# Performance work log

Hardware: AMD Instinct MI355X
Metric: run time of the kernel (lower is better)

The kernel has to match this reference:

```python
import jax, jax.numpy as jnp
import numpy as np

L, U, D_IN, D_OUT, B = 6, 256, 784, 10, 32768  # num_layers, units, input_dim, output_dim, batch


def setup_inputs() -> dict:
    key = jax.random.key(0)
    ks = jax.random.split(key, 7)
    s = jnp.float32(0.05)  # keras 'random_normal' initializer stddev
    return {
        "x": jax.random.normal(ks[0], (B, D_IN), jnp.float32),
        "W_in": jax.random.normal(ks[1], (D_IN, U), jnp.float32) * s,
        "b_in": jax.random.normal(ks[2], (U,), jnp.float32) * s,
        "B0": jax.random.normal(ks[3], (L, U, U), jnp.float32) * s,   # per-layer B0
        "q": jax.random.normal(ks[4], (L, U), jnp.float32) * s,       # per-layer q
        "W_out": jax.random.normal(ks[5], (U, D_OUT), jnp.float32) * s,
        "b_out": jax.random.normal(ks[6], (D_OUT,), jnp.float32) * s,
    }


def reference(x, W_in, b_in, B0, q, W_out, b_out):
    u = W_in.shape[1]
    v0 = (x @ W_in + b_in).T          # (u, B)
    v1 = jnp.tanh(v0)                  # activation of layer 0 applied once before the loop

    def step(carry, params):
        v0, v1 = carry
        B0_l, q_l = params
        z = jnp.zeros((u, u), B0_l.dtype)
        # skew-symmetric block system [[0, B0], [-B0^T, 0]]
        A = jnp.block([[z, B0_l], [-B0_l.T, z]])           # (2u, 2u)
        rhs = jnp.concatenate([v0 + q_l[:, None], v1], 0)   # (2u, B)
        sol = jnp.linalg.solve(A, rhs)
        return (sol[:u], sol[u:]), None

    (v0, v1), _ = jax.lax.scan(step, (v0, v1), (B0, q))
    return v0.T @ W_out + b_out        # (B, D_OUT)
```

## Files before the change

### kernel.cpp

```cpp
#include <hip/hip_runtime.h>
#include <math.h>

#define NU      256
#define NLAYERS 6
#define NBATCH  32768
#define NDIN    784
#define NDOUT   10
#define NUSQ    65536

typedef unsigned short u16;
typedef __attribute__((ext_vector_type(8))) short s16x8;
typedef __attribute__((ext_vector_type(4))) float f32x4;

__device__ __forceinline__ u16 f2bf(float x) {
    union { float f; unsigned u; } a; a.f = x;
    const unsigned r = a.u + 0x7fffu + ((a.u >> 16) & 1u);
    return (u16)(r >> 16);
}
__device__ __forceinline__ float bf2f(u16 h) {
    union { unsigned u; float f; } a; a.u = ((unsigned)h) << 16; return a.f;
}

__device__ __forceinline__ void gl_lds16(const u16* g, u16* l) {
    __builtin_amdgcn_global_load_lds(
        (const __attribute__((address_space(1))) void*)g,
        (__attribute__((address_space(3))) void*)l, 16, 0, 0);
}

#define COL_CASES(BODY) \
    case 0:  BODY(0);  break; case 1:  BODY(1);  break; \
    case 2:  BODY(2);  break; case 3:  BODY(3);  break; \
    case 4:  BODY(4);  break; case 5:  BODY(5);  break; \
    case 6:  BODY(6);  break; case 7:  BODY(7);  break; \
    case 8:  BODY(8);  break; case 9:  BODY(9);  break; \
    case 10: BODY(10); break; case 11: BODY(11); break; \
    case 12: BODY(12); break; case 13: BODY(13); break; \
    case 14: BODY(14); break; case 15: BODY(15); break; \
    case 16: BODY(16); break; case 17: BODY(17); break; \
    case 18: BODY(18); break; case 19: BODY(19); break; \
    case 20: BODY(20); break; case 21: BODY(21); break; \
    case 22: BODY(22); break; case 23: BODY(23); break; \
    case 24: BODY(24); break; case 25: BODY(25); break; \
    case 26: BODY(26); break; case 27: BODY(27); break; \
    case 28: BODY(28); break; case 29: BODY(29); break; \
    case 30: BODY(30); break; case 31: BODY(31); break;

__global__ __launch_bounds__(512, 2) void fused_inv_ingemm(
    const float* __restrict__ B0, const float* __restrict__ qg,
    u16* __restrict__ wnnh, u16* __restrict__ wnnl,
    u16* __restrict__ wnth, u16* __restrict__ wntl,
    float* __restrict__ bq,
    const float* __restrict__ X, const float* __restrict__ Win,
    const float* __restrict__ bin,
    u16* __restrict__ V0h, u16* __restrict__ V0l,
    u16* __restrict__ V1h, u16* __restrict__ V1l)
{
    __shared__ __align__(16) float colv[2][256];
    __shared__ int   s_p[2];
    __shared__ float s_pv[2];
    __shared__ int   pivrow[256];
    __shared__ int   ilogrow[256];
    __shared__ float qs[256];
    __shared__ float part[8][256];
    __shared__ __align__(16) float As[16][128];
    __shared__ __align__(16) float Bs[16][128];

    const int tid = threadIdx.x;

    if (blockIdx.x < NLAYERS) {
        const int layer = blockIdx.x;
        const int ct = tid & 63;
        const int wv = tid >> 6;

        float a[32][4];
        const float* Ablk = B0 + (size_t)layer * NU * NU;
#pragma unroll
        for (int j = 0; j < 4; ++j) {
            const float* rp = Ablk + (size_t)(ct*4 + j)*NU + wv*32;
#pragma unroll
            for (int i = 0; i < 32; i += 4) {
                const float4 v = *(const float4*)(rp + i);
                a[i+0][j] = v.x; a[i+1][j] = v.y; a[i+2][j] = v.z; a[i+3][j] = v.w;
            }
        }

        int used = 0;

        for (int k = 0; k < 256; ++k) {
            const int wvk = k >> 5, ikk = k & 31, buf = k & 1;

            if (wv == wvk) {
                float c0, c1, c2, c3;
#define EXT(I) { c0 = a[I][0]; c1 = a[I][1]; c2 = a[I][2]; c3 = a[I][3]; }
                switch (ikk) { COL_CASES(EXT) }
#undef EXT
                float ba = -1.0f, bv = 1.0f; int br = 0;
                {
                    float av;
                    av = (used & 1) ? -1.0f : fabsf(c0);
                    if (av > ba) { ba = av; bv = c0; br = ct*4 + 0; }
                    av = (used & 2) ? -1.0f : fabsf(c1);
                    if (av > ba) { ba = av; bv = c1; br = ct*4 + 1; }
                    av = (used & 4) ? -1.0f : fabsf(c2);
                    if (av > ba) { ba = av; bv = c2; br = ct*4 + 2; }
                    av = (used & 8) ? -1.0f : fabsf(c3);
                    if (av > ba) { ba = av; bv = c3; br = ct*4 + 3; }
                }
#pragma unroll
                for (int off = 32; off > 0; off >>= 1) {
                    const float oa = __shfl_down(ba, off);
                    const float ov = __shfl_down(bv, off);
                    const int   orr = __shfl_down(br, off);
                    if (oa > ba) { ba = oa; bv = ov; br = orr; }
                }
                float4 cw; cw.x = c0; cw.y = c1; cw.z = c2; cw.w = c3;
                *(float4*)(&colv[buf][ct*4]) = cw;
                if (ct == 0) {
                    s_p[buf] = br;
                    s_pv[buf] = 1.0f / bv;
                    pivrow[k] = br;
                }
            }
            __syncthreads();

            const int   p      = __builtin_amdgcn_readfirstlane(s_p[buf]);
            const float pivinv = s_pv[buf];
            const int ctp = p >> 2, jp = p & 3;

            const float4 dv = *(const float4*)(&colv[buf][ct*4]);

            float t[32];
#define SEL(J) { _Pragma("unroll") for (int i = 0; i < 32; ++i) t[i] = a[i][J]; }
            switch (jp) {
                case 0: SEL(0) break; case 1: SEL(1) break;
                case 2: SEL(2) break; default: SEL(3) break;
            }
#undef SEL
            float prw[32];
#pragma unroll
            for (int i = 0; i < 32; ++i) prw[i] = __shfl(t[i], ctp) * pivinv;

            if (wv == wvk) {
#define ZCOL(I) { prw[I] = pivinv; a[I][0] = 0.0f; a[I][1] = 0.0f; a[I][2] = 0.0f; a[I][3] = 0.0f; }
                switch (ikk) { COL_CASES(ZCOL) }
#undef ZCOL
            }

            const float d0 = -dv.x, d1 = -dv.y, d2 = -dv.z, d3 = -dv.w;
#pragma unroll
            for (int i = 0; i < 32; ++i) {
                const float pw = prw[i];
                a[i][0] = fmaf(d0, pw, a[i][0]);
                a[i][1] = fmaf(d1, pw, a[i][1]);
                a[i][2] = fmaf(d2, pw, a[i][2]);
                a[i][3] = fmaf(d3, pw, a[i][3]);
            }

            const bool mine = (ct == ctp);
#define OWR(J) { _Pragma("unroll") for (int i = 0; i < 32; ++i) a[i][J] = mine ? prw[i] : a[i][J]; }
            switch (jp) {
                case 0: OWR(0) break; case 1: OWR(1) break;
                case 2: OWR(2) break; default: OWR(3) break;
            }
#undef OWR
            if (mine) used |= (1 << jp);
        }
        __syncthreads();

        if (tid < 256) { ilogrow[pivrow[tid]] = tid; qs[tid] = qg[(size_t)layer*NU + tid]; }
        __syncthreads();

        {
            float s0=0.f, s1=0.f, s2=0.f, s3=0.f;
#pragma unroll
            for (int i = 0; i < 32; ++i) {
                const float qq = qs[pivrow[wv*32 + i]];
                s0 = fmaf(a[i][0], qq, s0);
                s1 = fmaf(a[i][1], qq, s1);
                s2 = fmaf(a[i][2], qq, s2);
                s3 = fmaf(a[i][3], qq, s3);
            }
            part[wv][ct*4+0] = s0; part[wv][ct*4+1] = s1;
            part[wv][ct*4+2] = s2; part[wv][ct*4+3] = s3;
        }
        __syncthreads();
        if (tid < 256) {
            float s = 0.f;
#pragma unroll
            for (int w2 = 0; w2 < 8; ++w2) s += part[w2][tid];
            bq[(size_t)layer*NU + ilogrow[tid]] = s;
        }

        u16* nh = wnnh + (size_t)layer*NUSQ; u16* nl = wnnl + (size_t)layer*NUSQ;
        u16* th = wnth + (size_t)layer*NUSQ; u16* tl = wntl + (size_t)layer*NUSQ;
#pragma unroll
        for (int j = 0; j < 4; ++j) {
            const int r = ilogrow[ct*4 + j];
#pragma unroll
            for (int i = 0; i < 32; ++i) {
                const int c = pivrow[wv*32 + i];
                const float v = a[i][j];
                const u16 h  = f2bf(v);
                const u16 lo = f2bf(v - bf2f(h));
                th[(size_t)r*NU + c] = h;  tl[(size_t)r*NU + c] = lo;
                nh[(size_t)c*NU + r] = h;  nl[(size_t)c*NU + r] = lo;
            }
        }
        return;
    }

    if (tid >= 256) return;

    const int bid = blockIdx.x - NLAYERS;
    const int m0 = (bid & 255) * 128;
    const int n0 = (bid >> 8) * 128;
    const int t  = tid;
    const int tx = t & 15, ty = t >> 4;
    const int K = NDIN;

    float acc[8][8];
#pragma unroll
    for (int i = 0; i < 8; ++i)
#pragma unroll
        for (int j = 0; j < 8; ++j) acc[i][j] = 0.0f;

    const int am = t >> 1;
    const int ak = (t & 1) * 8;
    const int bk = t >> 4;
    const int bn = (t & 15) * 8;

    for (int k0 = 0; k0 < K; k0 += 16) {
        const float* Ap = X + (size_t)(m0 + am)*K + (k0 + ak);
        const float4 a0 = *(const float4*)(Ap);
        const float4 a1 = *(const float4*)(Ap + 4);
        As[ak+0][am] = a0.x; As[ak+1][am] = a0.y; As[ak+2][am] = a0.z; As[ak+3][am] = a0.w;
        As[ak+4][am] = a1.x; As[ak+5][am] = a1.y; As[ak+6][am] = a1.z; As[ak+7][am] = a1.w;
        const float* Bp = Win + (size_t)(k0 + bk)*NU + (n0 + bn);
        const float4 b0 = *(const float4*)(Bp);
        const float4 b1 = *(const float4*)(Bp + 4);
        *(float4*)(&Bs[bk][bn])   = b0;
        *(float4*)(&Bs[bk][bn+4]) = b1;
        __syncthreads();
#pragma unroll
        for (int kk = 0; kk < 16; ++kk) {
            float af[8], bf[8];
            *(float4*)(af)   = *(const float4*)(&As[kk][ty*8]);
            *(float4*)(af+4) = *(const float4*)(&As[kk][ty*8+4]);
            *(float4*)(bf)   = *(const float4*)(&Bs[kk][tx*8]);
            *(float4*)(bf+4) = *(const float4*)(&Bs[kk][tx*8+4]);
#pragma unroll
            for (int i = 0; i < 8; ++i)
#pragma unroll
                for (int j = 0; j < 8; ++j)
                    acc[i][j] = fmaf(af[i], bf[j], acc[i][j]);
        }
        __syncthreads();
    }

#pragma unroll
    for (int i = 0; i < 8; ++i) {
        const size_t row = m0 + ty*8 + i;
        s16x8 vh, vl, th2, tl2;
#pragma unroll
        for (int j = 0; j < 8; ++j) {
            const float v = acc[i][j] + bin[n0 + tx*8 + j];
            const u16 h  = f2bf(v);
            vh[j] = (short)h; vl[j] = (short)f2bf(v - bf2f(h));
            const float tv = tanhf(v);
            const u16 h2 = f2bf(tv);
            th2[j] = (short)h2; tl2[j] = (short)f2bf(tv - bf2f(h2));
        }
        const size_t o = row*NU + n0 + tx*8;
        *(s16x8*)&V0h[o] = vh; *(s16x8*)&V0l[o] = vl;
        *(s16x8*)&V1h[o] = th2; *(s16x8*)&V1l[o] = tl2;
    }
}

__global__ __launch_bounds__(256, 2) void gemm_mfma(
    const u16* __restrict__ Ah, const u16* __restrict__ Al,
    const u16* __restrict__ Bh, const u16* __restrict__ Bl,
    u16* __restrict__ Ch, u16* __restrict__ Cl,
    const float* __restrict__ bias, const float alpha)
{
    __shared__ __align__(16) u16 lAh[128*32], lAl[128*32], lBh[128*32], lBl[128*32];
    const int t    = threadIdx.x;
    const int lane = t & 63;
    const int w    = t >> 6;
    const int wr = w >> 1, wc = w & 1;
    const int qd = lane >> 4, l15 = lane & 15;
    const int m0 = blockIdx.x * 128, n0 = blockIdx.y * 128;

    const int srow = t >> 2;
    const int skc  = (t & 3) * 8;

    f32x4 acc[4][4];
    const f32x4 z = {0.f, 0.f, 0.f, 0.f};
#pragma unroll
    for (int i = 0; i < 4; ++i)
#pragma unroll
        for (int j = 0; j < 4; ++j) acc[i][j] = z;

    for (int k0 = 0; k0 < NU; k0 += 32) {
#pragma unroll
        for (int half = 0; half < 2; ++half) {
            const int rr = srow + half*64;
            const size_t ga = (size_t)(m0 + rr)*NU + k0 + skc;
            const size_t gb = (size_t)(n0 + rr)*NU + k0 + skc;
            const int lo = rr*32 + skc;
            gl_lds16(Ah + ga, &lAh[lo]);
            gl_lds16(Al + ga, &lAl[lo]);
            gl_lds16(Bh + gb, &lBh[lo]);
            gl_lds16(Bl + gb, &lBl[lo]);
        }
        __syncthreads();

        s16x8 ah[4], al[4], bh[4], bl[4];
#pragma unroll
        for (int mt = 0; mt < 4; ++mt) {
            const int off = (wr*64 + mt*16 + l15)*32 + qd*8;
            ah[mt] = *(const s16x8*)&lAh[off];
            al[mt] = *(const s16x8*)&lAl[off];
        }
#pragma unroll
        for (int nt = 0; nt < 4; ++nt) {
            const int off = (wc*64 + nt*16 + l15)*32 + qd*8;
            bh[nt] = *(const s16x8*)&lBh[off];
            bl[nt] = *(const s16x8*)&lBl[off];
        }
#pragma unroll
        for (int mt = 0; mt < 4; ++mt)
#pragma unroll
            for (int nt = 0; nt < 4; ++nt) {
                acc[mt][nt] = __builtin_amdgcn_mfma_f32_16x16x32_bf16(ah[mt], bh[nt], acc[mt][nt], 0, 0, 0);
                acc[mt][nt] = __builtin_amdgcn_mfma_f32_16x16x32_bf16(ah[mt], bl[nt], acc[mt][nt], 0, 0, 0);
                acc[mt][nt] = __builtin_amdgcn_mfma_f32_16x16x32_bf16(al[mt], bh[nt], acc[mt][nt], 0, 0, 0);
            }
        __syncthreads();
    }

#pragma unroll
    for (int mt = 0; mt < 4; ++mt) {
#pragma unroll
        for (int nt = 0; nt < 4; ++nt) {
            const int col = n0 + wc*64 + nt*16 + l15;
            const float bb = bias ? bias[col] : 0.0f;
#pragma unroll
            for (int r = 0; r < 4; ++r) {
                const int row = m0 + wr*64 + mt*16 + qd*4 + r;
                const float v = alpha*acc[mt][nt][r] + bb;
                const u16 h  = f2bf(v);
                const u16 lo = f2bf(v - bf2f(h));
                const size_t o = (size_t)row*NU + col;
                Ch[o] = h; Cl[o] = lo;
            }
        }
    }
}

__global__ __launch_bounds__(256) void out_gemm(
    const u16* __restrict__ V0h, const u16* __restrict__ V0l,
    const float* __restrict__ Wout,
    const float* __restrict__ bout, float* __restrict__ out)
{
    __shared__ float Ws[NU*NDOUT];
    const int t = threadIdx.x;
    for (int i = t; i < NU*NDOUT; i += 256) Ws[i] = Wout[i];
    __syncthreads();
    const int lane = t & 63;
    const int wv = t >> 6;
    const int row = blockIdx.x*4 + wv;
    float acc[NDOUT];
#pragma unroll
    for (int j = 0; j < NDOUT; ++j) acc[j] = 0.0f;
#pragma unroll
    for (int s = 0; s < 4; ++s) {
        const int k = lane + 64*s;
        const size_t o = (size_t)row*NU + k;
        const float v = bf2f(V0h[o]) + bf2f(V0l[o]);
#pragma unroll
        for (int j = 0; j < NDOUT; ++j) acc[j] = fmaf(v, Ws[k*NDOUT + j], acc[j]);
    }
#pragma unroll
    for (int off = 32; off > 0; off >>= 1) {
#pragma unroll
        for (int j = 0; j < NDOUT; ++j) acc[j] += __shfl_down(acc[j], off);
    }
    if (lane == 0) {
#pragma unroll
        for (int j = 0; j < NDOUT; ++j) out[(size_t)row*NDOUT + j] = acc[j] + bout[j];
    }
}

extern "C" void kernel_launch(void* const* d_in, const int* in_sizes, int n_in,
                              void* d_out, int out_size, void* d_ws, size_t ws_size,
                              hipStream_t stream)
{
    const float* x    = (const float*)d_in[0];
    const float* Win  = (const float*)d_in[1];
    const float* bin  = (const float*)d_in[2];
    const float* B0   = (const float*)d_in[3];
    const float* q    = (const float*)d_in[4];
    const float* Wout = (const float*)d_in[5];
    const float* bout = (const float*)d_in[6];
    float* out = (float*)d_out;

    u16* wnnh = (u16*)d_ws;
    u16* wnnl = wnnh + (size_t)NLAYERS*NUSQ;
    u16* wnth = wnnl + (size_t)NLAYERS*NUSQ;
    u16* wntl = wnth + (size_t)NLAYERS*NUSQ;
    float* bq = (float*)(wntl + (size_t)NLAYERS*NUSQ);
    u16* pl   = (u16*)(bq + NLAYERS*NU);
    const size_t PSZ = (size_t)NBATCH*NU;
    u16* sAh = pl;           u16* sAl = sAh + PSZ;
    u16* sBh = sAl + PSZ;    u16* sBl = sBh + PSZ;
    u16* sCh = sBl + PSZ;    u16* sCl = sCh + PSZ;

    fused_inv_ingemm<<<NLAYERS + 512, 512, 0, stream>>>(
        B0, q, wnnh, wnnl, wnth, wntl, bq,
        x, Win, bin, sAh, sAl, sBh, sBl);

    const dim3 ggrid(NBATCH/128, NU/128);

    u16 *v0h = sAh, *v0l = sAl, *v1h = sBh, *v1l = sBl, *frh = sCh, *frl = sCl;
    for (int l = 0; l < NLAYERS; ++l) {
        const size_t wo = (size_t)l*NUSQ;
        gemm_mfma<<<ggrid, 256, 0, stream>>>(v1h, v1l, wnnh + wo, wnnl + wo,
                                             frh, frl, nullptr, -1.0f);
        gemm_mfma<<<ggrid, 256, 0, stream>>>(v0h, v0l, wnth + wo, wntl + wo,
                                             v1h, v1l, bq + (size_t)l*NU, 1.0f);
        u16* t0 = v0h; u16* t1 = v0l;
        v0h = frh; v0l = frl; frh = t0; frl = t1;
    }
    out_gemm<<<NBATCH/4, 256, 0, stream>>>(v0h, v0l, Wout, bout, out);
}
```

Before: 1.012 ms.

## Pipeline next pivot search with current update in Gauss-Jordan inversion

Restructures the in-register Gauss-Jordan elimination so the wave owning the next column computes that column's updated values and pivot during the current step (lookahead). This removes the serial pivot search that sat before the barrier on the critical path. Pivot search now uses a packed abs|row key with xor-shuffle umax, and pivot-row broadcast uses readlane instead of shfl. It also folds pivinv into the multipliers. Packing the row index into the low mantissa bits slightly coarsens pivot selection, which could change which pivot is chosen.

```diff
diff --git a/kernel.cpp b/kernel.cpp
--- a/kernel.cpp
+++ b/kernel.cpp
@@ -25,6 +25,23 @@
     __builtin_amdgcn_global_load_lds(
         (const __attribute__((address_space(1))) void*)g,
         (__attribute__((address_space(3))) void*)l, 16, 0, 0);
+}
+
+__device__ __forceinline__ float rlf(float v, int lane) {
+    return __int_as_float(__builtin_amdgcn_readlane(__float_as_int(v), lane));
+}
+
+__device__ __forceinline__ unsigned pkey(float v, int row) {
+    return (__float_as_uint(fabsf(v)) & 0xFFFFFF00u) | (unsigned)row;
+}
+
+__device__ __forceinline__ unsigned wave_umax64(unsigned key) {
+#pragma unroll
+    for (int off = 1; off < 64; off <<= 1) {
+        const unsigned o = (unsigned)__shfl_xor((int)key, off);
+        key = key > o ? key : o;
+    }
+    return key;
 }
 
 #define COL_CASES(BODY) \
@@ -86,84 +103,103 @@
 
         int used = 0;
 
+        if (wv == 0) {
+            const float c0 = a[0][0], c1 = a[0][1], c2 = a[0][2], c3 = a[0][3];
+            unsigned key = pkey(c0, ct*4 + 0);
+            unsigned k1  = pkey(c1, ct*4 + 1); key = key > k1 ? key : k1;
+            unsigned k2  = pkey(c2, ct*4 + 2); key = key > k2 ? key : k2;
+            unsigned k3  = pkey(c3, ct*4 + 3); key = key > k3 ? key : k3;
+            key = wave_umax64(key);
+            const int pn = __builtin_amdgcn_readfirstlane((int)(key & 255u));
+            float bv;
+            switch (pn & 3) {
+                case 0: bv = rlf(c0, pn >> 2); break;
+                case 1: bv = rlf(c1, pn >> 2); break;
+                case 2: bv = rlf(c2, pn >> 2); break;
+                default: bv = rlf(c3, pn >> 2); break;
+            }
+            float4 cw; cw.x = c0; cw.y = c1; cw.z = c2; cw.w = c3;
+            *(float4*)(&colv[0][ct*4]) = cw;
+            if (ct == 0) { s_p[0] = pn; s_pv[0] = 1.0f / bv; pivrow[0] = pn; }
+        }
+        __syncthreads();
+
         for (int k = 0; k < 256; ++k) {
-            const int wvk = k >> 5, ikk = k & 31, buf = k & 1;
-
-            if (wv == wvk) {
-                float c0, c1, c2, c3;
-#define EXT(I) { c0 = a[I][0]; c1 = a[I][1]; c2 = a[I][2]; c3 = a[I][3]; }
-                switch (ikk) { COL_CASES(EXT) }
-#undef EXT
-                float ba = -1.0f, bv = 1.0f; int br = 0;
-                {
-                    float av;
-                    av = (used & 1) ? -1.0f : fabsf(c0);
-                    if (av > ba) { ba = av; bv = c0; br = ct*4 + 0; }
-                    av = (used & 2) ? -1.0f : fabsf(c1);
-                    if (av > ba) { ba = av; bv = c1; br = ct*4 + 1; }
-                    av = (used & 4) ? -1.0f : fabsf(c2);
-                    if (av > ba) { ba = av; bv = c2; br = ct*4 + 2; }
-                    av = (used & 8) ? -1.0f : fabsf(c3);
-                    if (av > ba) { ba = av; bv = c3; br = ct*4 + 3; }
-                }
-#pragma unroll
-                for (int off = 32; off > 0; off >>= 1) {
-                    const float oa = __shfl_down(ba, off);
-                    const float ov = __shfl_down(bv, off);
-                    const int   orr = __shfl_down(br, off);
-                    if (oa > ba) { ba = oa; bv = ov; br = orr; }
-                }
-                float4 cw; cw.x = c0; cw.y = c1; cw.z = c2; cw.w = c3;
-                *(float4*)(&colv[buf][ct*4]) = cw;
-                if (ct == 0) {
-                    s_p[buf] = br;
-                    s_pv[buf] = 1.0f / bv;
-                    pivrow[k] = br;
-                }
-            }
-            __syncthreads();
-
-            const int   p      = __builtin_amdgcn_readfirstlane(s_p[buf]);
+            const int buf = k & 1, nbuf = buf ^ 1;
+            const int p        = __builtin_amdgcn_readfirstlane(s_p[buf]);
             const float pivinv = s_pv[buf];
             const int ctp = p >> 2, jp = p & 3;
+            const bool mine = (ct == ctp);
 
             const float4 dv = *(const float4*)(&colv[buf][ct*4]);
-
-            float t[32];
-#define SEL(J) { _Pragma("unroll") for (int i = 0; i < 32; ++i) t[i] = a[i][J]; }
+            const float d0 = -dv.x * pivinv, d1 = -dv.y * pivinv,
+                        d2 = -dv.z * pivinv, d3 = -dv.w * pivinv;
+
+            if (mine) used |= (1 << jp);
+
+            const int kn = k + 1;
+            if (kn < 256 && wv == (kn >> 5)) {
+                const int inx = kn & 31;
+                float s_inx = 0.0f, t0 = 0.0f, t1 = 0.0f, t2 = 0.0f, t3 = 0.0f;
+#define AH(I) { switch (jp) { \
+                    case 0: s_inx = rlf(a[I][0], ctp); break; \
+                    case 1: s_inx = rlf(a[I][1], ctp); break; \
+                    case 2: s_inx = rlf(a[I][2], ctp); break; \
+                    default: s_inx = rlf(a[I][3], ctp); break; } \
+                t0 = fmaf(d0, s_inx, a[I][0]); \
+                t1 = fmaf(d1, s_inx, a[I][1]); \
+                t2 = fmaf(d2, s_inx, a[I][2]); \
+                t3 = fmaf(d3, s_inx, a[I][3]); }
+                switch (inx) { COL_CASES(AH) }
+#undef AH
+                if (mine) {
+                    const float pv2 = s_inx * pivinv;
+                    switch (jp) {
+                        case 0: t0 = pv2; break; case 1: t1 = pv2; break;
+                        case 2: t2 = pv2; break; default: t3 = pv2; break;
+                    }
+                }
+                unsigned key = (used & 1) ? 0u : pkey(t0, ct*4 + 0);
+                unsigned q1  = (used & 2) ? 0u : pkey(t1, ct*4 + 1); key = key > q1 ? key : q1;
+                unsigned q2  = (used & 4) ? 0u : pkey(t2, ct*4 + 2); key = key > q2 ? key : q2;
+                unsigned q3  = (used & 8) ? 0u : pkey(t3, ct*4 + 3); key = key > q3 ? key : q3;
+                key = wave_umax64(key);
+                const int pn2 = __builtin_amdgcn_readfirstlane((int)(key & 255u));
+                float bv2;
+                switch (pn2 & 3) {
+                    case 0: bv2 = rlf(t0, pn2 >> 2); break;
+                    case 1: bv2 = rlf(t1, pn2 >> 2); break;
+                    case 2: bv2 = rlf(t2, pn2 >> 2); break;
+                    default: bv2 = rlf(t3, pn2 >> 2); break;
+                }
+                float4 cw; cw.x = t0; cw.y = t1; cw.z = t2; cw.w = t3;
+                *(float4*)(&colv[nbuf][ct*4]) = cw;
+                if (ct == 0) { s_p[nbuf] = pn2; s_pv[nbuf] = 1.0f / bv2; pivrow[kn] = pn2; }
+            }
+
+#define UPDJ(J) { _Pragma("unroll") for (int i = 0; i < 32; ++i) { \
+                const float s = rlf(a[i][J], ctp); \
+                a[i][0] = fmaf(d0, s, a[i][0]); \
+                a[i][1] = fmaf(d1, s, a[i][1]); \
+                a[i][2] = fmaf(d2, s, a[i][2]); \
+                a[i][3] = fmaf(d3, s, a[i][3]); \
+                a[i][J] = mine ? s * pivinv : a[i][J]; } }
             switch (jp) {
-                case 0: SEL(0) break; case 1: SEL(1) break;
-                case 2: SEL(2) break; default: SEL(3) break;
-            }
-#undef SEL
-            float prw[32];
-#pragma unroll
-            for (int i = 0; i < 32; ++i) prw[i] = __shfl(t[i], ctp) * pivinv;
-
-            if (wv == wvk) {
-#define ZCOL(I) { prw[I] = pivinv; a[I][0] = 0.0f; a[I][1] = 0.0f; a[I][2] = 0.0f; a[I][3] = 0.0f; }
-                switch (ikk) { COL_CASES(ZCOL) }
-#undef ZCOL
-            }
-
-            const float d0 = -dv.x, d1 = -dv.y, d2 = -dv.z, d3 = -dv.w;
-#pragma unroll
-            for (int i = 0; i < 32; ++i) {
-                const float pw = prw[i];
-                a[i][0] = fmaf(d0, pw, a[i][0]);
-                a[i][1] = fmaf(d1, pw, a[i][1]);
-                a[i][2] = fmaf(d2, pw, a[i][2]);
-                a[i][3] = fmaf(d3, pw, a[i][3]);
-            }
-
-            const bool mine = (ct == ctp);
-#define OWR(J) { _Pragma("unroll") for (int i = 0; i < 32; ++i) a[i][J] = mine ? prw[i] : a[i][J]; }
-            switch (jp) {
-                case 0: OWR(0) break; case 1: OWR(1) break;
-                case 2: OWR(2) break; default: OWR(3) break;
-            }
-#undef OWR
-            if (mine) used |= (1 << jp);
+                case 0: UPDJ(0) break; case 1: UPDJ(1) break;
+                case 2: UPDJ(2) break; default: UPDJ(3) break;
+            }
+#undef UPDJ
+
+            if (wv == (k >> 5)) {
+                const int ikk = k & 31;
+#define FIXK(I) { a[I][0] = d0; a[I][1] = d1; a[I][2] = d2; a[I][3] = d3; \
+                  if (mine) { switch (jp) { \
+                      case 0: a[I][0] = pivinv; break; case 1: a[I][1] = pivinv; break; \
+                      case 2: a[I][2] = pivinv; break; default: a[I][3] = pivinv; break; } } }
+                switch (ikk) { COL_CASES(FIXK) }
+#undef FIXK
+            }
+            __syncthreads();
         }
         __syncthreads();
 
```

New measurement: 1.145 ms. +13.2%, slower.

## Block Gauss-Jordan pivot steps in panels of 32 to cut barriers

Applied to the files above, without the earlier changes.

The in-place Gauss-Jordan inversion of each layer's B0 matrix moves from one block-wide barrier per pivot to a panel scheme. The owning wave factors 32 pivot columns on its own and records the update vectors in LDS. The other waves then apply all 32 rank-1 updates after a single barrier. Pivot search now packs |value| and row index into one unsigned key reduced with xor-shuffles, and row broadcasts use readlane instead of shfl. This removes most __syncthreads calls and serialization in the 6-block inversion phase. In exchange, the owning wave works alone during each panel, LDS use grows (32x256 floats), and the truncated pivot key may pick slightly different pivots.

```diff
diff --git a/kernel.cpp b/kernel.cpp
--- a/kernel.cpp
+++ b/kernel.cpp
@@ -25,6 +25,23 @@
     __builtin_amdgcn_global_load_lds(
         (const __attribute__((address_space(1))) void*)g,
         (__attribute__((address_space(3))) void*)l, 16, 0, 0);
+}
+
+__device__ __forceinline__ float rlf(float v, int lane) {
+    return __int_as_float(__builtin_amdgcn_readlane(__float_as_int(v), lane));
+}
+
+__device__ __forceinline__ unsigned pkey(float v, int row) {
+    return (__float_as_uint(fabsf(v)) & 0xFFFFFF00u) | (unsigned)row;
+}
+
+__device__ __forceinline__ unsigned wave_umax64(unsigned key) {
+#pragma unroll
+    for (int off = 1; off < 64; off <<= 1) {
+        const unsigned o = (unsigned)__shfl_xor((int)key, off);
+        key = key > o ? key : o;
+    }
+    return key;
 }
 
 #define COL_CASES(BODY) \
@@ -55,9 +72,7 @@
     u16* __restrict__ V0h, u16* __restrict__ V0l,
     u16* __restrict__ V1h, u16* __restrict__ V1l)
 {
-    __shared__ __align__(16) float colv[2][256];
-    __shared__ int   s_p[2];
-    __shared__ float s_pv[2];
+    __shared__ __align__(16) float g_lds[32][256];
     __shared__ int   pivrow[256];
     __shared__ int   ilogrow[256];
     __shared__ float qs[256];
@@ -86,86 +101,92 @@
 
         int used = 0;
 
-        for (int k = 0; k < 256; ++k) {
-            const int wvk = k >> 5, ikk = k & 31, buf = k & 1;
-
-            if (wv == wvk) {
-                float c0, c1, c2, c3;
+        for (int p = 0; p < 8; ++p) {
+            const int k0 = p * 32;
+
+            if (wv == p) {
+                for (int kk = 0; kk < 32; ++kk) {
+                    float c0, c1, c2, c3;
 #define EXT(I) { c0 = a[I][0]; c1 = a[I][1]; c2 = a[I][2]; c3 = a[I][3]; }
-                switch (ikk) { COL_CASES(EXT) }
+                    switch (kk) { COL_CASES(EXT) }
 #undef EXT
-                float ba = -1.0f, bv = 1.0f; int br = 0;
-                {
-                    float av;
-                    av = (used & 1) ? -1.0f : fabsf(c0);
-                    if (av > ba) { ba = av; bv = c0; br = ct*4 + 0; }
-                    av = (used & 2) ? -1.0f : fabsf(c1);
-                    if (av > ba) { ba = av; bv = c1; br = ct*4 + 1; }
-                    av = (used & 4) ? -1.0f : fabsf(c2);
-                    if (av > ba) { ba = av; bv = c2; br = ct*4 + 2; }
-                    av = (used & 8) ? -1.0f : fabsf(c3);
-                    if (av > ba) { ba = av; bv = c3; br = ct*4 + 3; }
+                    unsigned key = (used & 1) ? 0u : pkey(c0, ct*4 + 0);
+                    unsigned q1  = (used & 2) ? 0u : pkey(c1, ct*4 + 1); key = key > q1 ? key : q1;
+                    unsigned q2  = (used & 4) ? 0u : pkey(c2, ct*4 + 2); key = key > q2 ? key : q2;
+                    unsigned q3  = (used & 8) ? 0u : pkey(c3, ct*4 + 3); key = key > q3 ? key : q3;
+                    key = wave_umax64(key);
+                    const int pn  = __builtin_amdgcn_readfirstlane((int)(key & 255u));
+                    const int ctp = pn >> 2, jp = pn & 3;
+                    float bv;
+                    switch (jp) {
+                        case 0: bv = rlf(c0, ctp); break;
+                        case 1: bv = rlf(c1, ctp); break;
+                        case 2: bv = rlf(c2, ctp); break;
+                        default: bv = rlf(c3, ctp); break;
+                    }
+                    const float pivinv = 1.0f / bv;
+                    const bool mine = (ct == ctp);
+
+                    float g0 = c0*pivinv, g1 = c1*pivinv, g2 = c2*pivinv, g3 = c3*pivinv;
+                    if (mine) {
+                        switch (jp) {
+                            case 0: g0 = 1.0f - pivinv; break;
+                            case 1: g1 = 1.0f - pivinv; break;
+                            case 2: g2 = 1.0f - pivinv; break;
+                            default: g3 = 1.0f - pivinv; break;
+                        }
+                    }
+                    float4 gw; gw.x = g0; gw.y = g1; gw.z = g2; gw.w = g3;
+                    *(float4*)(&g_lds[kk][ct*4]) = gw;
+                    if (ct == 0) pivrow[k0 + kk] = pn;
+
+#define UPD(J) { _Pragma("unroll") for (int j = 0; j < 32; ++j) { \
+                        const float s = rlf(a[j][J], ctp); \
+                        a[j][0] = fmaf(-g0, s, a[j][0]); \
+                        a[j][1] = fmaf(-g1, s, a[j][1]); \
+                        a[j][2] = fmaf(-g2, s, a[j][2]); \
+                        a[j][3] = fmaf(-g3, s, a[j][3]); } }
+                    switch (jp) {
+                        case 0: UPD(0) break; case 1: UPD(1) break;
+                        case 2: UPD(2) break; default: UPD(3) break;
+                    }
+#undef UPD
+                    float t0 = -g0, t1 = -g1, t2 = -g2, t3 = -g3;
+                    if (mine) {
+                        switch (jp) {
+                            case 0: t0 = pivinv; break; case 1: t1 = pivinv; break;
+                            case 2: t2 = pivinv; break; default: t3 = pivinv; break;
+                        }
+                    }
+#define CKO(I) { a[I][0] = t0; a[I][1] = t1; a[I][2] = t2; a[I][3] = t3; }
+                    switch (kk) { COL_CASES(CKO) }
+#undef CKO
+                    if (mine) used |= (1 << jp);
                 }
-#pragma unroll
-                for (int off = 32; off > 0; off >>= 1) {
-                    const float oa = __shfl_down(ba, off);
-                    const float ov = __shfl_down(bv, off);
-                    const int   orr = __shfl_down(br, off);
-                    if (oa > ba) { ba = oa; bv = ov; br = orr; }
+            }
+            __syncthreads();
+
+            if (wv != p) {
+                for (int kk = 0; kk < 32; ++kk) {
+                    const int rk = __builtin_amdgcn_readfirstlane(pivrow[k0 + kk]);
+                    const int ctp = rk >> 2, jp = rk & 3;
+                    const float4 gv = *(const float4*)(&g_lds[kk][ct*4]);
+#define UPDU(J) { _Pragma("unroll") for (int j = 0; j < 32; ++j) { \
+                        const float s = rlf(a[j][J], ctp); \
+                        a[j][0] = fmaf(-gv.x, s, a[j][0]); \
+                        a[j][1] = fmaf(-gv.y, s, a[j][1]); \
+                        a[j][2] = fmaf(-gv.z, s, a[j][2]); \
+                        a[j][3] = fmaf(-gv.w, s, a[j][3]); } }
+                    switch (jp) {
+                        case 0: UPDU(0) break; case 1: UPDU(1) break;
+                        case 2: UPDU(2) break; default: UPDU(3) break;
+                    }
+#undef UPDU
+                    if (ct == ctp) used |= (1 << jp);
                 }
-                float4 cw; cw.x = c0; cw.y = c1; cw.z = c2; cw.w = c3;
-                *(float4*)(&colv[buf][ct*4]) = cw;
-                if (ct == 0) {
-                    s_p[buf] = br;
-                    s_pv[buf] = 1.0f / bv;
-                    pivrow[k] = br;
-                }
             }
             __syncthreads();
-
-            const int   p      = __builtin_amdgcn_readfirstlane(s_p[buf]);
-            const float pivinv = s_pv[buf];
-            const int ctp = p >> 2, jp = p & 3;
-
-            const float4 dv = *(const float4*)(&colv[buf][ct*4]);
-
-            float t[32];
-#define SEL(J) { _Pragma("unroll") for (int i = 0; i < 32; ++i) t[i] = a[i][J]; }
-            switch (jp) {
-                case 0: SEL(0) break; case 1: SEL(1) break;
-                case 2: SEL(2) break; default: SEL(3) break;
-            }
-#undef SEL
-            float prw[32];
-#pragma unroll
-            for (int i = 0; i < 32; ++i) prw[i] = __shfl(t[i], ctp) * pivinv;
-
-            if (wv == wvk) {
-#define ZCOL(I) { prw[I] = pivinv; a[I][0] = 0.0f; a[I][1] = 0.0f; a[I][2] = 0.0f; a[I][3] = 0.0f; }
-                switch (ikk) { COL_CASES(ZCOL) }
-#undef ZCOL
-            }
-
-            const float d0 = -dv.x, d1 = -dv.y, d2 = -dv.z, d3 = -dv.w;
-#pragma unroll
-            for (int i = 0; i < 32; ++i) {
-                const float pw = prw[i];
-                a[i][0] = fmaf(d0, pw, a[i][0]);
-                a[i][1] = fmaf(d1, pw, a[i][1]);
-                a[i][2] = fmaf(d2, pw, a[i][2]);
-                a[i][3] = fmaf(d3, pw, a[i][3]);
-            }
-
-            const bool mine = (ct == ctp);
-#define OWR(J) { _Pragma("unroll") for (int i = 0; i < 32; ++i) a[i][J] = mine ? prw[i] : a[i][J]; }
-            switch (jp) {
-                case 0: OWR(0) break; case 1: OWR(1) break;
-                case 2: OWR(2) break; default: OWR(3) break;
-            }
-#undef OWR
-            if (mine) used |= (1 << jp);
-        }
-        __syncthreads();
+        }
 
         if (tid < 256) { ilogrow[pivrow[tid]] = tid; qs[tid] = qg[(size_t)layer*NU + tid]; }
         __syncthreads();
```

Measured after the change: 1.748 ms. +72.7%, slower.
